# Kernel optimization log

Hardware: AMD Instinct MI355X
Metric: run time of the kernel (lower is better)

Reference implementation:

```python
import jax, jax.numpy as jnp
import numpy as np

B, L, D = 16, 2048, 128
GROUP = 16
NG = L // GROUP  # number of groups per batch
ALPHA = 0.5


def setup_inputs() -> dict:
    key = jax.random.key(0)
    k0, k1, k2 = jax.random.split(key, 3)
    x = jax.random.normal(k0, (B, L, D), dtype=jnp.float32)
    # per-batch permutation = gather indices (each position used exactly once)
    group_tensor = jax.vmap(lambda k: jax.random.permutation(k, L))(
        jax.random.split(k1, B)).astype(jnp.int32)
    ctxlens = jnp.full((B,), L, dtype=jnp.int32)
    W = jax.random.normal(k2, (2 * D,), dtype=jnp.float32) * (1.0 / np.sqrt(D))
    norm_alpha = jnp.ones((2,), dtype=jnp.float32)
    norm_gamma = jnp.ones((2 * D,), dtype=jnp.float32)
    norm_beta = jnp.zeros((2 * D,), dtype=jnp.float32)
    return {"x": x, "group_tensor": group_tensor, "ctxlens": ctxlens, "W": W,
            "norm_alpha": norm_alpha, "norm_gamma": norm_gamma, "norm_beta": norm_beta}


def _leaky_relu(v):
    return jnp.where(v >= 0, v, 0.01 * v)


def _ncn_forward(x, group_tensor, ctxlens, W, norm_alpha, norm_gamma, norm_beta):
    Bd, Ld, Dd = x.shape
    ng = Ld // GROUP
    Wi, Wj = W[:Dd], W[Dd:]
    a1, a2 = norm_alpha[0], norm_alpha[1]
    g1, g2 = norm_gamma[:Dd], norm_gamma[Dd:]
    b1, b2 = norm_beta[:Dd], norm_beta[Dd:]

    # gather x by group indices -> [B, NG, GROUP, D]
    xg = jnp.take_along_axis(x, group_tensor[:, :, None].astype(jnp.int32), axis=1)
    xg = xg.reshape(Bd, ng, GROUP, Dd)

    def step(carry, j):
        xi, xa = carry  # each [B, NG, GROUP, D]
        xj = jax.lax.dynamic_slice_in_dim(xi, j, 1, axis=2)  # [B, NG, 1, D]
        sim = jnp.einsum('bgnd,d->bgn', xi, Wi) \
            + jnp.einsum('bgd,d->bg', xj[:, :, 0, :], Wj)[:, :, None]  # [B,NG,GROUP]
        T = ALPHA * xi + (1.0 - ALPHA) * sim[..., None] * xj
        T_norm = g1 * jnp.tanh(a1 * T) + b1
        Fv = _leaky_relu(T_norm)
        xa = xa + Fv                               # ya = xa + F
        xi = xi + g2 * jnp.tanh(a2 * xa) + b2      # yi = xi + norm2(ya)
        return (xi, xa), None

    (yi, ya), _ = jax.lax.scan(step, (xg, jnp.zeros_like(xg)), jnp.arange(GROUP))

    # kernel only processes/stores a group if its start offset < ctxlen
    valid = (jnp.arange(ng, dtype=jnp.int32) * GROUP)[None, :] < ctxlens[:, None]
    yi = jnp.where(valid[:, :, None, None], yi, 0.0).reshape(Bd, Ld, Dd)
    ya = jnp.where(valid[:, :, None, None], ya, 0.0).reshape(Bd, Ld, Dd)

    # scatter back to original positions
    bidx = jnp.arange(Bd)[:, None]
    yi_out = jnp.zeros_like(x).at[bidx, group_tensor].set(yi)
    ya_out = jnp.zeros_like(x).at[bidx, group_tensor].set(ya)
    return yi_out, ya_out


def reference(x, group_tensor, ctxlens, W, norm_alpha, norm_gamma, norm_beta):
    return _ncn_forward(x, group_tensor, ctxlens, W, norm_alpha, norm_gamma, norm_beta)
```

## Files before the change

kernel.cpp:

```cpp
#include <hip/hip_runtime.h>

#define B_ 16
#define L_ 2048
#define D_ 128
#define GROUP_ 16
#define NG_ (L_ / GROUP_)
#define LOG2E_ 1.44269504088896340736f

template<int CTRL>
__device__ __forceinline__ float dpp_add(float v) {
    int x = __builtin_amdgcn_update_dpp(0, __float_as_int(v), CTRL, 0xF, 0xF, false);
    return v + __int_as_float(x);
}
__device__ __forceinline__ float row16_sum(float v) {
    v = dpp_add<0xB1>(v);
    v = dpp_add<0x4E>(v);
    v = dpp_add<0x141>(v);
    v = dpp_add<0x140>(v);
    return v;
}

__device__ __forceinline__ void rcp8(const float d[8], float r[8]) {
    float p[8];
    p[0] = d[0];
#pragma unroll
    for (int k = 1; k < 8; ++k) p[k] = p[k - 1] * d[k];
    float R = __builtin_amdgcn_rcpf(p[7]);
#pragma unroll
    for (int k = 7; k >= 1; --k) { r[k] = p[k - 1] * R; R *= d[k]; }
    r[0] = R;
}

__global__ __launch_bounds__(256, 4) void ncn_kernel(
    const float* __restrict__ x,
    const int*   __restrict__ gt,
    const int*   __restrict__ ctxlens,
    const float* __restrict__ W,
    const float* __restrict__ nalpha,
    const float* __restrict__ ngamma,
    const float* __restrict__ nbeta,
    float* __restrict__ out)
{
    const int blk = blockIdx.x;
    const int b   = blk >> 7;
    const int g   = blk & (NG_ - 1);
    const int tid = threadIdx.x;
    const int row = tid >> 4;
    const int rl  = tid & 15;
    const int d0  = rl << 3;

    __shared__ float s_xj[2][D_];
    __shared__ float s_sjW[2];

    const float a1 = nalpha[0];
    const float a2 = nalpha[1];
    const float ca = -a1 * LOG2E_;
    const float S  = -2.0f * a2 * LOG2E_;
    const bool  selMin = (S < 0.0f);

    float Wi[8], Wj[8], G1S[8], B1S[8], G2[8], B2[8];
    {
        float g1r[8], b1r[8], g2r[8], b2r[8];
        *(float4*)&Wi[0]  = *(const float4*)(W + d0);
        *(float4*)&Wi[4]  = *(const float4*)(W + d0 + 4);
        *(float4*)&Wj[0]  = *(const float4*)(W + D_ + d0);
        *(float4*)&Wj[4]  = *(const float4*)(W + D_ + d0 + 4);
        *(float4*)&g1r[0] = *(const float4*)(ngamma + d0);
        *(float4*)&g1r[4] = *(const float4*)(ngamma + d0 + 4);
        *(float4*)&g2r[0] = *(const float4*)(ngamma + D_ + d0);
        *(float4*)&g2r[4] = *(const float4*)(ngamma + D_ + d0 + 4);
        *(float4*)&b1r[0] = *(const float4*)(nbeta + d0);
        *(float4*)&b1r[4] = *(const float4*)(nbeta + d0 + 4);
        *(float4*)&b2r[0] = *(const float4*)(nbeta + D_ + d0);
        *(float4*)&b2r[4] = *(const float4*)(nbeta + D_ + d0 + 4);
#pragma unroll
        for (int k = 0; k < 8; ++k) {
            G1S[k] = S * 2.0f * g1r[k];
            B1S[k] = S * (b1r[k] - g1r[k]);
            G2[k]  = 2.0f * g2r[k];
            B2[k]  = b2r[k] - g2r[k];
        }
    }
#pragma unroll
    for (int k = 0; k < 8; ++k) {
        asm volatile("" : "+v"(Wi[k]));
        asm volatile("" : "+v"(Wj[k]));
        asm volatile("" : "+v"(G1S[k]));
        asm volatile("" : "+v"(B1S[k]));
        asm volatile("" : "+v"(G2[k]));
        asm volatile("" : "+v"(B2[k]));
    }

    const int l   = g * GROUP_ + row;
    const int tok = gt[b * L_ + l];
    const float* xp = x + ((size_t)(b * L_ + tok)) * D_ + d0;

    float xi[8], za[8];
    *(float4*)&xi[0] = *(const float4*)xp;
    *(float4*)&xi[4] = *(const float4*)(xp + 4);
#pragma unroll
    for (int k = 0; k < 8; ++k) za[k] = 0.0f;

    if (row == 0) {
        *(float4*)&s_xj[0][d0]     = *(float4*)&xi[0];
        *(float4*)&s_xj[0][d0 + 4] = *(float4*)&xi[4];
        float w = 0.0f;
#pragma unroll
        for (int k = 0; k < 8; ++k) w = fmaf(xi[k], Wj[k], w);
        w = row16_sum(w);
        if (rl == 0) s_sjW[0] = w;
    }

    for (int j = 0; j < GROUP_; ++j) {
        __syncthreads();
        const int p = j & 1;

        float xjv[8];
        *(float4*)&xjv[0] = *(const float4*)&s_xj[p][d0];
        *(float4*)&xjv[4] = *(const float4*)&s_xj[p][d0 + 4];
        const float sjW = s_sjW[p];

        float s = 0.0f;
#pragma unroll
        for (int k = 0; k < 8; ++k) s = fmaf(xi[k], Wi[k], s);
        s = row16_sum(s);
        const float sim = s + sjW;
        const float cb  = ca * sim;

        float darr[8], r1[8];
#pragma unroll
        for (int k = 0; k < 8; ++k) {
            float u = fmaf(ca, xi[k], cb * xjv[k]);
            u = fminf(u, 15.0f);
            darr[k] = 1.0f + __builtin_amdgcn_exp2f(u);
        }
        rcp8(darr, r1);

#pragma unroll
        for (int k = 0; k < 8; ++k) {
            float tnS = fmaf(G1S[k], r1[k], B1S[k]);
            float alt = 0.01f * tnS;
            float FvS = selMin ? fminf(tnS, alt) : fmaxf(tnS, alt);
            za[k] += FvS;
            float z = fminf(za[k], 15.0f);
            darr[k] = 1.0f + __builtin_amdgcn_exp2f(z);
        }
        rcp8(darr, r1);

#pragma unroll
        for (int k = 0; k < 8; ++k)
            xi[k] += fmaf(G2[k], r1[k], B2[k]);

        if (row == j + 1) {
            *(float4*)&s_xj[p ^ 1][d0]     = *(float4*)&xi[0];
            *(float4*)&s_xj[p ^ 1][d0 + 4] = *(float4*)&xi[4];
            float w = 0.0f;
#pragma unroll
            for (int k = 0; k < 8; ++k) w = fmaf(xi[k], Wj[k], w);
            w = row16_sum(w);
            if (rl == 0) s_sjW[p ^ 1] = w;
        }
    }

    const float invS = 1.0f / S;
    float xa[8];
#pragma unroll
    for (int k = 0; k < 8; ++k) xa[k] = za[k] * invS;

    const bool valid = (g * GROUP_) < ctxlens[b];
    if (!valid) {
#pragma unroll
        for (int k = 0; k < 8; ++k) { xi[k] = 0.0f; xa[k] = 0.0f; }
    }

    float* o1 = out + ((size_t)(b * L_ + tok)) * D_ + d0;
    float* o2 = o1 + (size_t)B_ * L_ * D_;
    *(float4*)o1       = *(float4*)&xi[0];
    *(float4*)(o1 + 4) = *(float4*)&xi[4];
    *(float4*)o2       = *(float4*)&xa[0];
    *(float4*)(o2 + 4) = *(float4*)&xa[4];
}

extern "C" void kernel_launch(void* const* d_in, const int* in_sizes, int n_in,
                              void* d_out, int out_size, void* d_ws, size_t ws_size,
                              hipStream_t stream) {
    const float* x  = (const float*)d_in[0];
    const int*   gt = (const int*)d_in[1];
    const int*   cl = (const int*)d_in[2];
    const float* W  = (const float*)d_in[3];
    const float* na = (const float*)d_in[4];
    const float* ng = (const float*)d_in[5];
    const float* nb = (const float*)d_in[6];
    float* out = (float*)d_out;

    ncn_kernel<<<B_ * NG_, 256, 0, stream>>>(x, gt, cl, W, na, ng, nb, out);
}
```

Measured before the change: 122.6 us.

## Replace per-step block barriers with LDS flag spin-waits and per-step xj slots

Drops the `__syncthreads` at each of the 16 scan steps. Each step's xj row now goes into its own LDS slot, published by a block-scope fence and a volatile flag that consumer waves poll with `s_sleep`. The Wj·xj term is now computed redundantly by every row inside the fused dot-product reduction, instead of by the producer row with a separate shared scalar. The empty asm statements that pinned the constant parameters in VGPRs are removed, which may change register allocation. Spin-waiting with sleep can add wake-up latency to a chain that is serial anyway.

```diff
diff --git a/kernel.cpp b/kernel.cpp
--- a/kernel.cpp
+++ b/kernel.cpp
@@ -49,8 +49,10 @@
     const int rl  = tid & 15;
     const int d0  = rl << 3;
 
-    __shared__ float s_xj[2][D_];
-    __shared__ float s_sjW[2];
+    __shared__ float s_xj[GROUP_][D_];
+    __shared__ int   s_flag[GROUP_];
+
+    if (tid < GROUP_) s_flag[tid] = 0;
 
     const float a1 = nalpha[0];
     const float a2 = nalpha[1];
@@ -81,15 +83,6 @@
             B2[k]  = b2r[k] - g2r[k];
         }
     }
-#pragma unroll
-    for (int k = 0; k < 8; ++k) {
-        asm volatile("" : "+v"(Wi[k]));
-        asm volatile("" : "+v"(Wj[k]));
-        asm volatile("" : "+v"(G1S[k]));
-        asm volatile("" : "+v"(B1S[k]));
-        asm volatile("" : "+v"(G2[k]));
-        asm volatile("" : "+v"(B2[k]));
-    }
 
     const int l   = g * GROUP_ + row;
     const int tok = gt[b * L_ + l];
@@ -101,31 +94,31 @@
 #pragma unroll
     for (int k = 0; k < 8; ++k) za[k] = 0.0f;
 
+    __syncthreads();
+
+    volatile int* vflag = (volatile int*)s_flag;
+
     if (row == 0) {
         *(float4*)&s_xj[0][d0]     = *(float4*)&xi[0];
         *(float4*)&s_xj[0][d0 + 4] = *(float4*)&xi[4];
-        float w = 0.0f;
-#pragma unroll
-        for (int k = 0; k < 8; ++k) w = fmaf(xi[k], Wj[k], w);
-        w = row16_sum(w);
-        if (rl == 0) s_sjW[0] = w;
+        __threadfence_block();
+        if (rl == 0) vflag[0] = 1;
     }
 
     for (int j = 0; j < GROUP_; ++j) {
-        __syncthreads();
-        const int p = j & 1;
+        while (vflag[j] == 0) { __builtin_amdgcn_s_sleep(1); }
 
         float xjv[8];
-        *(float4*)&xjv[0] = *(const float4*)&s_xj[p][d0];
-        *(float4*)&xjv[4] = *(const float4*)&s_xj[p][d0 + 4];
-        const float sjW = s_sjW[p];
+        *(float4*)&xjv[0] = *(const float4*)&s_xj[j][d0];
+        *(float4*)&xjv[4] = *(const float4*)&s_xj[j][d0 + 4];
 
         float s = 0.0f;
 #pragma unroll
         for (int k = 0; k < 8; ++k) s = fmaf(xi[k], Wi[k], s);
+#pragma unroll
+        for (int k = 0; k < 8; ++k) s = fmaf(xjv[k], Wj[k], s);
         s = row16_sum(s);
-        const float sim = s + sjW;
-        const float cb  = ca * sim;
+        const float cb = ca * s;
 
         float darr[8], r1[8];
 #pragma unroll
@@ -152,13 +145,10 @@
             xi[k] += fmaf(G2[k], r1[k], B2[k]);
 
         if (row == j + 1) {
-            *(float4*)&s_xj[p ^ 1][d0]     = *(float4*)&xi[0];
-            *(float4*)&s_xj[p ^ 1][d0 + 4] = *(float4*)&xi[4];
-            float w = 0.0f;
-#pragma unroll
-            for (int k = 0; k < 8; ++k) w = fmaf(xi[k], Wj[k], w);
-            w = row16_sum(w);
-            if (rl == 0) s_sjW[p ^ 1] = w;
+            *(float4*)&s_xj[j + 1][d0]     = *(float4*)&xi[0];
+            *(float4*)&s_xj[j + 1][d0 + 4] = *(float4*)&xi[4];
+            __threadfence_block();
+            if (rl == 0) vflag[j + 1] = 1;
         }
     }
 
```

Measured after the change: 124.6 us. About the same (+1.6%).
